# Performance work log

Measured on AMD Instinct MI355X. Metric: run time of the kernel, lower is better.

Reference implementation:

```python
import jax, jax.numpy as jnp
import numpy as np

B, T, J = 64, 1024, 22
PARENTS = [0, 0, 1, 2, 3, 0, 5, 6, 7, 0, 9, 10, 11, 12, 11, 14, 15, 16, 11, 18, 19, 20]
SPARSE_JOINTS = [0, 4, 8, 13, 17, 21]
EE = tuple(SPARSE_JOINTS[1:])                       # end effectors (sparse_joints[1:])
NO_SPARSE = tuple(j for j in range(J) if j not in SPARSE_JOINTS)
LAMBDA_EE, LAMBDA_EE_REG = 1.0, 0.1
IDENT_DQ = np.array([1, 0, 0, 0, 0, 0, 0, 0], dtype=np.float32)


def _qconj(q):
    return q * jnp.array([1.0, -1.0, -1.0, -1.0], q.dtype)


def _qmul(a, b):
    aw, ax, ay, az = a[..., 0], a[..., 1], a[..., 2], a[..., 3]
    bw, bx, by, bz = b[..., 0], b[..., 1], b[..., 2], b[..., 3]
    return jnp.stack([
        aw * bw - ax * bx - ay * by - az * bz,
        aw * bx + ax * bw + ay * bz - az * by,
        aw * by - ax * bz + ay * bw + az * bx,
        aw * bz + ax * by - ay * bx + az * bw], axis=-1)


def _qrot(q, v):
    # rotate vector v by unit quaternion q
    qv = q[..., 1:]
    t = 2.0 * jnp.cross(qv, v)
    return v + q[..., :1] * t + jnp.cross(qv, t)


def _qmat(q):
    w, x, y, z = q[..., 0], q[..., 1], q[..., 2], q[..., 3]
    m = jnp.stack([
        1 - 2 * (y * y + z * z), 2 * (x * y - w * z), 2 * (x * z + w * y),
        2 * (x * y + w * z), 1 - 2 * (x * x + z * z), 2 * (y * z - w * x),
        2 * (x * z - w * y), 2 * (y * z + w * x), 1 - 2 * (x * x + y * y)], axis=-1)
    return m.reshape(m.shape[:-1] + (3, 3))


def _denorm_to_dq(x, mean, std, set_root_identity):
    # x: (B, J*8, T) channel-major dual quats -> (B, T, J, 8)
    x = x * std[None, :, None] + mean[None, :, None]
    if set_root_identity:
        x = x.at[:, :8, :].set(jnp.asarray(IDENT_DQ, x.dtype)[None, :, None])
    b, c, t = x.shape
    return x.reshape(b, c // 8, 8, t).transpose(0, 3, 1, 2)


def _local_rot_from_dq(dq):
    # skeleton_from_dual_quat: real part = global rotation; make local via parent gather
    qr = dq[..., :4]
    qr = qr / jnp.linalg.norm(qr, axis=-1, keepdims=True)
    parent = jnp.asarray(PARENTS)
    local = _qmul(_qconj(qr[:, :, parent, :]), qr)   # (B,T,J,4)
    # forward_ik overwrites root local rotation with identity
    local = local.at[:, :, 0, :].set(jnp.array([1.0, 0.0, 0.0, 0.0], dq.dtype))
    return local


def _fk(local_rot, offsets):
    # fk_2: sequential parent-indexed propagation; root global pos is zeros
    rots = [local_rot[:, :, 0]]
    poss = [jnp.zeros(local_rot.shape[:2] + (3,), local_rot.dtype)]
    for j in range(1, J):
        p = PARENTS[j]
        rots.append(_qmul(rots[p], local_rot[:, :, j]))
        poss.append(_qrot(rots[p], offsets[j]) + poss[p])
    grot = jnp.stack(rots, axis=2)          # (B,T,J,4)
    pos = jnp.stack(poss, axis=2)           # (B,T,J,3)
    return pos, _qmat(grot)                  # positions, (B,T,J,3,3) rot matrices


def setup_inputs() -> dict:
    key = jax.random.key(0)
    ks = jax.random.split(key, 7)
    C = J * 8
    return {
        "input": jax.random.normal(ks[0], (B, C, T), jnp.float32),
        "input_ik": jax.random.normal(ks[1], (B, C - 8, T), jnp.float32),
        "input_decoder": jax.random.normal(ks[2], (B, C, T), jnp.float32),
        "target": jax.random.normal(ks[3], (B, C, T), jnp.float32),
        "mean_dqs": 0.1 * jax.random.normal(ks[4], (C,), jnp.float32),
        "std_dqs": 0.5 + 0.5 * jax.random.uniform(ks[5], (C,), jnp.float32),
        "offsets": jax.random.normal(ks[6], (J, 3), jnp.float32),
    }


def reference(input, input_ik, input_decoder, target, mean_dqs, std_dqs, offsets):
    # prepend identity-slot for the root (8 zero channels), then denormalize
    dq_ik = jnp.concatenate([jnp.zeros_like(input_ik[:, :8, :]), input_ik], axis=1)
    dq_ik = _denorm_to_dq(dq_ik, mean_dqs, std_dqs, True)
    dq_dec = _denorm_to_dq(input_decoder, mean_dqs, std_dqs, True)
    dq_tgt = _denorm_to_dq(target, mean_dqs, std_dqs, False)

    r_ik = _local_rot_from_dq(dq_ik)
    r_dec = _local_rot_from_dq(dq_dec)
    r_tgt = _local_rot_from_dq(dq_tgt)

    pos, rm = _fk(r_ik, offsets)
    tpos, trm = _fk(r_tgt, offsets)
    dpos, drm = _fk(r_dec, offsets)

    ee = jnp.asarray(EE)
    ns = jnp.asarray(NO_SPARSE)
    mse = lambda a, b: jnp.mean((a - b) ** 2)
    loss_ee = mse(pos[:, :, ee], tpos[:, :, ee]) + mse(rm[:, :, ee], trm[:, :, ee])
    loss_reg = mse(dpos[:, :, ns], pos[:, :, ns]) + mse(drm[:, :, ns], rm[:, :, ns])
    return loss_ee * LAMBDA_EE + loss_reg * LAMBDA_EE_REG
```

## Files before the change

### kernel.cpp

```cpp
#include <hip/hip_runtime.h>


#define T_DIM 1024

struct Q { float w, x, y, z; };
struct V3 { float x, y, z; };
struct St { Q rot; V3 pos; };

__device__ __forceinline__ Q qmul(const Q a, const Q b) {
    Q r;
    r.w = a.w*b.w - a.x*b.x - a.y*b.y - a.z*b.z;
    r.x = a.w*b.x + a.x*b.w + a.y*b.z - a.z*b.y;
    r.y = a.w*b.y - a.x*b.z + a.y*b.w + a.z*b.x;
    r.z = a.w*b.z + a.x*b.y - a.y*b.x + a.z*b.w;
    return r;
}

__device__ __forceinline__ V3 qrot(const Q q, const V3 v) {
    float tx = 2.f*(q.y*v.z - q.z*v.y);
    float ty = 2.f*(q.z*v.x - q.x*v.z);
    float tz = 2.f*(q.x*v.y - q.y*v.x);
    V3 r;
    r.x = v.x + q.w*tx + (q.y*tz - q.z*ty);
    r.y = v.y + q.w*ty + (q.z*tx - q.x*tz);
    r.z = v.z + q.w*tz + (q.x*ty - q.y*tx);
    return r;
}

__device__ __forceinline__ void qmat(const Q q, float m[9]) {
    float xx=q.x*q.x, yy=q.y*q.y, zz=q.z*q.z;
    float xy=q.x*q.y, xz=q.x*q.z, yz=q.y*q.z;
    float wx=q.w*q.x, wy=q.w*q.y, wz=q.w*q.z;
    m[0]=1.f-2.f*(yy+zz); m[1]=2.f*(xy-wz);     m[2]=2.f*(xz+wy);
    m[3]=2.f*(xy+wz);     m[4]=1.f-2.f*(xx+zz); m[5]=2.f*(yz-wx);
    m[6]=2.f*(xz-wy);     m[7]=2.f*(yz+wx);     m[8]=1.f-2.f*(xx+yy);
}

__device__ __forceinline__ float rmdiff2(const Q a, const Q b) {
    float ma[9], mb[9];
    qmat(a, ma); qmat(b, mb);
    float s = 0.f;
#pragma unroll
    for (int i = 0; i < 9; ++i) { float d = ma[i]-mb[i]; s += d*d; }
    return s;
}

__device__ __forceinline__ float pdiff2(const V3 a, const V3 b) {
    float dx=a.x-b.x, dy=a.y-b.y, dz=a.z-b.z;
    return dx*dx+dy*dy+dz*dz;
}

__device__ __forceinline__ V3 v3add(const V3 a, const V3 b) {
    return V3{a.x+b.x, a.y+b.y, a.z+b.z};
}

__device__ __forceinline__ Q mkq(const float r[4], const int c0,
                                 const float* __restrict__ mean,
                                 const float* __restrict__ stdv) {
    Q q;
    q.w = r[0]*stdv[c0+0] + mean[c0+0];
    q.x = r[1]*stdv[c0+1] + mean[c0+1];
    q.y = r[2]*stdv[c0+2] + mean[c0+2];
    q.z = r[3]*stdv[c0+3] + mean[c0+3];
    float inv = rsqrtf(q.w*q.w + q.x*q.x + q.y*q.y + q.z*q.z);
    q.w*=inv; q.x*=inv; q.y*=inv; q.z*=inv;
    return q;
}

template<int J0, int N>
__device__ __forceinline__ void prefetch_chain(
    const float* __restrict__ ikp, const float* __restrict__ dep,
    const float* __restrict__ tgp,
    float (*ikr)[4], float (*der)[4], float (*tgr)[4])
{
#pragma unroll
    for (int jj = 0; jj < N; ++jj) {
        const int j = J0 + jj;
#pragma unroll
        for (int c = 0; c < 4; ++c) {
            ikr[jj][c] = ikp[((j-1)*8 + c)*T_DIM];
            der[jj][c] = dep[(j*8 + c)*T_DIM];
            tgr[jj][c] = tgp[(j*8 + c)*T_DIM];
        }
    }
}

template<int J, bool EE>
__device__ __forceinline__ void stepr(
    St& sik, St& sde, St& stg,
    const float ikr[4], const float der[4], const float tgr[4],
    const float* __restrict__ mean, const float* __restrict__ stdv,
    const float* __restrict__ offs, const Q q0c,
    float& aep, float& aer, float& arp, float& arr)
{
    const int c0 = J*8;
    Q qik = mkq(ikr, c0, mean, stdv);
    Q qde = mkq(der, c0, mean, stdv);
    Q qtg = mkq(tgr, c0, mean, stdv);
    V3 off = { offs[3*J], offs[3*J+1], offs[3*J+2] };
    V3 pik = v3add(qrot(sik.rot, off), sik.pos);
    V3 pde = v3add(qrot(sde.rot, off), sde.pos);
    V3 ptg = v3add(qrot(stg.rot, off), stg.pos);
    Q rtg = qmul(q0c, qtg);
    if (EE) {
        aep += pdiff2(pik, ptg);
        aer += rmdiff2(qik, rtg);
    } else {
        arp += pdiff2(pde, pik);
        arr += rmdiff2(qde, qik);
    }
    sik.rot = qik; sik.pos = pik;
    sde.rot = qde; sde.pos = pde;
    stg.rot = rtg; stg.pos = ptg;
}

__global__ __launch_bounds__(256, 1) void fk_loss_kernel(
    const float* __restrict__ ik, const float* __restrict__ dec,
    const float* __restrict__ tgt, const float* __restrict__ mean,
    const float* __restrict__ stdv, const float* __restrict__ offs,
    float* __restrict__ out)
{
    __shared__ float swred[4];
    const int tid = threadIdx.x;
    const int p = blockIdx.x * 256 + tid;
    const int b = p >> 10;
    const int t = p & 1023;
    const float* ikp = ik  + (size_t)b * (168*1024) + t;
    const float* dep = dec + (size_t)b * (176*1024) + t;
    const float* tgp = tgt + (size_t)b * (176*1024) + t;

    float aep=0.f, aer=0.f, arp=0.f, arr=0.f;

    float Aik[4][4], Ade[4][4], Atg[4][4];
    float Bik[4][4], Bde[4][4], Btg[4][4];
    float Cik[5][4], Cde[5][4], Ctg[5][4];
    float Dik[4][4], Dde[4][4], Dtg[4][4];
    float Eik[4][4], Ede[4][4], Etg[4][4];
    float rq0[4];

#pragma unroll
    for (int c = 0; c < 4; ++c) rq0[c] = tgp[c*T_DIM];
    prefetch_chain<1,4>(ikp, dep, tgp, Aik, Ade, Atg);
    prefetch_chain<5,4>(ikp, dep, tgp, Bik, Bde, Btg);

    Q q0 = mkq(rq0, 0, mean, stdv);
    const Q q0c = { q0.w, -q0.x, -q0.y, -q0.z };
    const St root = { {1.f,0.f,0.f,0.f}, {0.f,0.f,0.f} };
    St sik, sde, stg;

    sik = root; sde = root; stg = root;
    stepr<1,false>(sik,sde,stg, Aik[0],Ade[0],Atg[0], mean,stdv,offs, q0c, aep,aer,arp,arr);
    stepr<2,false>(sik,sde,stg, Aik[1],Ade[1],Atg[1], mean,stdv,offs, q0c, aep,aer,arp,arr);
    stepr<3,false>(sik,sde,stg, Aik[2],Ade[2],Atg[2], mean,stdv,offs, q0c, aep,aer,arp,arr);
    stepr<4,true >(sik,sde,stg, Aik[3],Ade[3],Atg[3], mean,stdv,offs, q0c, aep,aer,arp,arr);

    prefetch_chain<9,5>(ikp, dep, tgp, Cik, Cde, Ctg);

    sik = root; sde = root; stg = root;
    stepr<5,false>(sik,sde,stg, Bik[0],Bde[0],Btg[0], mean,stdv,offs, q0c, aep,aer,arp,arr);
    stepr<6,false>(sik,sde,stg, Bik[1],Bde[1],Btg[1], mean,stdv,offs, q0c, aep,aer,arp,arr);
    stepr<7,false>(sik,sde,stg, Bik[2],Bde[2],Btg[2], mean,stdv,offs, q0c, aep,aer,arp,arr);
    stepr<8,true >(sik,sde,stg, Bik[3],Bde[3],Btg[3], mean,stdv,offs, q0c, aep,aer,arp,arr);

    prefetch_chain<14,4>(ikp, dep, tgp, Dik, Dde, Dtg);

    sik = root; sde = root; stg = root;
    stepr<9, false>(sik,sde,stg, Cik[0],Cde[0],Ctg[0], mean,stdv,offs, q0c, aep,aer,arp,arr);
    stepr<10,false>(sik,sde,stg, Cik[1],Cde[1],Ctg[1], mean,stdv,offs, q0c, aep,aer,arp,arr);
    stepr<11,false>(sik,sde,stg, Cik[2],Cde[2],Ctg[2], mean,stdv,offs, q0c, aep,aer,arp,arr);
    const St sik11 = sik, sde11 = sde, stg11 = stg;
    stepr<12,false>(sik,sde,stg, Cik[3],Cde[3],Ctg[3], mean,stdv,offs, q0c, aep,aer,arp,arr);
    stepr<13,true >(sik,sde,stg, Cik[4],Cde[4],Ctg[4], mean,stdv,offs, q0c, aep,aer,arp,arr);

    prefetch_chain<18,4>(ikp, dep, tgp, Eik, Ede, Etg);

    sik = sik11; sde = sde11; stg = stg11;
    stepr<14,false>(sik,sde,stg, Dik[0],Dde[0],Dtg[0], mean,stdv,offs, q0c, aep,aer,arp,arr);
    stepr<15,false>(sik,sde,stg, Dik[1],Dde[1],Dtg[1], mean,stdv,offs, q0c, aep,aer,arp,arr);
    stepr<16,false>(sik,sde,stg, Dik[2],Dde[2],Dtg[2], mean,stdv,offs, q0c, aep,aer,arp,arr);
    stepr<17,true >(sik,sde,stg, Dik[3],Dde[3],Dtg[3], mean,stdv,offs, q0c, aep,aer,arp,arr);

    sik = sik11; sde = sde11; stg = stg11;
    stepr<18,false>(sik,sde,stg, Eik[0],Ede[0],Etg[0], mean,stdv,offs, q0c, aep,aer,arp,arr);
    stepr<19,false>(sik,sde,stg, Eik[1],Ede[1],Etg[1], mean,stdv,offs, q0c, aep,aer,arp,arr);
    stepr<20,false>(sik,sde,stg, Eik[2],Ede[2],Etg[2], mean,stdv,offs, q0c, aep,aer,arp,arr);
    stepr<21,true >(sik,sde,stg, Eik[3],Ede[3],Etg[3], mean,stdv,offs, q0c, aep,aer,arp,arr);

    const float BT = 65536.f;
    float loss = aep * (1.0f/(BT*15.f))
               + aer * (1.0f/(BT*45.f))
               + arp * (0.1f/(BT*48.f))
               + arr * (0.1f/(BT*144.f));

#pragma unroll
    for (int o = 32; o > 0; o >>= 1) loss += __shfl_down(loss, o);
    if ((tid & 63) == 0) swred[tid >> 6] = loss;
    __syncthreads();
    if (tid == 0) {
        atomicAdd(out, swred[0]+swred[1]+swred[2]+swred[3]);
    }
}

extern "C" void kernel_launch(void* const* d_in, const int* in_sizes, int n_in,
                              void* d_out, int out_size, void* d_ws, size_t ws_size,
                              hipStream_t stream) {
    const float* ikx  = (const float*)d_in[1];
    const float* dec  = (const float*)d_in[2];
    const float* tgt  = (const float*)d_in[3];
    const float* mean = (const float*)d_in[4];
    const float* stdv = (const float*)d_in[5];
    const float* offs = (const float*)d_in[6];
    float* out = (float*)d_out;

    hipMemsetAsync(out, 0, sizeof(float), stream);
    fk_loss_kernel<<<256, 256, 0, stream>>>(ikx, dec, tgt, mean, stdv, offs, out);
}
```

Measured before the change: 173.0 us.

## Split FK loss into two thread roles and use closed-form rotation-matrix distance

Each block now has 512 threads: half compute the end-effector loss (ik vs target FK), the other half compute the regularizer (decoder vs ik FK). Each thread tracks two chains instead of three, which cuts register pressure and doubles the parallelism over the same 256 blocks. The ik chain is therefore computed twice, once per role. The 9-element rotation-matrix squared difference is replaced by the identity 8(1 - (a·b)^2) for unit quaternions, which drops the matrix construction.

```diff
diff --git a/kernel.cpp b/kernel.cpp
--- a/kernel.cpp
+++ b/kernel.cpp
@@ -27,22 +27,9 @@
     return r;
 }
 
-__device__ __forceinline__ void qmat(const Q q, float m[9]) {
-    float xx=q.x*q.x, yy=q.y*q.y, zz=q.z*q.z;
-    float xy=q.x*q.y, xz=q.x*q.z, yz=q.y*q.z;
-    float wx=q.w*q.x, wy=q.w*q.y, wz=q.w*q.z;
-    m[0]=1.f-2.f*(yy+zz); m[1]=2.f*(xy-wz);     m[2]=2.f*(xz+wy);
-    m[3]=2.f*(xy+wz);     m[4]=1.f-2.f*(xx+zz); m[5]=2.f*(yz-wx);
-    m[6]=2.f*(xz-wy);     m[7]=2.f*(yz+wx);     m[8]=1.f-2.f*(xx+yy);
-}
-
-__device__ __forceinline__ float rmdiff2(const Q a, const Q b) {
-    float ma[9], mb[9];
-    qmat(a, ma); qmat(b, mb);
-    float s = 0.f;
-#pragma unroll
-    for (int i = 0; i < 9; ++i) { float d = ma[i]-mb[i]; s += d*d; }
-    return s;
+__device__ __forceinline__ float rmdiff2u(const Q a, const Q b) {
+    float d = a.w*b.w + a.x*b.x + a.y*b.y + a.z*b.z;
+    return 8.f*(1.f - d*d);
 }
 
 __device__ __forceinline__ float pdiff2(const V3 a, const V3 b) {
@@ -68,136 +55,149 @@
 }
 
 template<int J0, int N>
-__device__ __forceinline__ void prefetch_chain(
-    const float* __restrict__ ikp, const float* __restrict__ dep,
-    const float* __restrict__ tgp,
-    float (*ikr)[4], float (*der)[4], float (*tgr)[4])
+__device__ __forceinline__ void pf2(
+    const float* __restrict__ xp, const float* __restrict__ yp,
+    float (*xr)[4], float (*yr)[4])
 {
 #pragma unroll
     for (int jj = 0; jj < N; ++jj) {
         const int j = J0 + jj;
 #pragma unroll
         for (int c = 0; c < 4; ++c) {
-            ikr[jj][c] = ikp[((j-1)*8 + c)*T_DIM];
-            der[jj][c] = dep[(j*8 + c)*T_DIM];
-            tgr[jj][c] = tgp[(j*8 + c)*T_DIM];
+            xr[jj][c] = xp[(j*8 + c)*T_DIM];
+            yr[jj][c] = yp[(j*8 + c)*T_DIM];
         }
     }
 }
 
-template<int J, bool EE>
-__device__ __forceinline__ void stepr(
-    St& sik, St& sde, St& stg,
-    const float ikr[4], const float der[4], const float tgr[4],
+template<int J, bool LOSS, bool PRE>
+__device__ __forceinline__ void step2(
+    St& sx, St& sy,
+    const float xr[4], const float yr[4],
     const float* __restrict__ mean, const float* __restrict__ stdv,
     const float* __restrict__ offs, const Q q0c,
-    float& aep, float& aer, float& arp, float& arr)
+    float& ap, float& ar)
 {
     const int c0 = J*8;
-    Q qik = mkq(ikr, c0, mean, stdv);
-    Q qde = mkq(der, c0, mean, stdv);
-    Q qtg = mkq(tgr, c0, mean, stdv);
+    Q qx = mkq(xr, c0, mean, stdv);
+    Q qy = mkq(yr, c0, mean, stdv);
+    if (PRE) qy = qmul(q0c, qy);
     V3 off = { offs[3*J], offs[3*J+1], offs[3*J+2] };
-    V3 pik = v3add(qrot(sik.rot, off), sik.pos);
-    V3 pde = v3add(qrot(sde.rot, off), sde.pos);
-    V3 ptg = v3add(qrot(stg.rot, off), stg.pos);
-    Q rtg = qmul(q0c, qtg);
-    if (EE) {
-        aep += pdiff2(pik, ptg);
-        aer += rmdiff2(qik, rtg);
-    } else {
-        arp += pdiff2(pde, pik);
-        arr += rmdiff2(qde, qik);
-    }
-    sik.rot = qik; sik.pos = pik;
-    sde.rot = qde; sde.pos = pde;
-    stg.rot = rtg; stg.pos = ptg;
-}
-
-__global__ __launch_bounds__(256, 1) void fk_loss_kernel(
+    V3 px = v3add(qrot(sx.rot, off), sx.pos);
+    V3 py = v3add(qrot(sy.rot, off), sy.pos);
+    if (LOSS) {
+        ap += pdiff2(px, py);
+        ar += rmdiff2u(qx, qy);
+    }
+    sx.rot = qx; sx.pos = px;
+    sy.rot = qy; sy.pos = py;
+}
+
+template<bool EEROLE>
+__device__ __forceinline__ void walk(
+    const float* __restrict__ xp, const float* __restrict__ yp,
+    const float* __restrict__ mean, const float* __restrict__ stdv,
+    const float* __restrict__ offs,
+    float& ap, float& ar)
+{
+    float Xa[4][4], Ya[4][4];
+    float Xb[4][4], Yb[4][4];
+    float Xc[5][4], Yc[5][4];
+    float Xd[4][4], Yd[4][4];
+    float Xe[4][4], Ye[4][4];
+    float rq0[4];
+
+    if (EEROLE) {
+#pragma unroll
+        for (int c = 0; c < 4; ++c) rq0[c] = yp[c*T_DIM];
+    }
+    pf2<1,4>(xp, yp, Xa, Ya);
+    pf2<5,4>(xp, yp, Xb, Yb);
+
+    Q q0c = {1.f, 0.f, 0.f, 0.f};
+    if (EEROLE) {
+        Q q0 = mkq(rq0, 0, mean, stdv);
+        q0c = { q0.w, -q0.x, -q0.y, -q0.z };
+    }
+    const St root = { {1.f,0.f,0.f,0.f}, {0.f,0.f,0.f} };
+    St sx, sy;
+
+    sx = root; sy = root;
+    step2<1, !EEROLE, EEROLE>(sx,sy, Xa[0],Ya[0], mean,stdv,offs,q0c, ap,ar);
+    step2<2, !EEROLE, EEROLE>(sx,sy, Xa[1],Ya[1], mean,stdv,offs,q0c, ap,ar);
+    step2<3, !EEROLE, EEROLE>(sx,sy, Xa[2],Ya[2], mean,stdv,offs,q0c, ap,ar);
+    step2<4,  EEROLE, EEROLE>(sx,sy, Xa[3],Ya[3], mean,stdv,offs,q0c, ap,ar);
+
+    pf2<9,5>(xp, yp, Xc, Yc);
+
+    sx = root; sy = root;
+    step2<5, !EEROLE, EEROLE>(sx,sy, Xb[0],Yb[0], mean,stdv,offs,q0c, ap,ar);
+    step2<6, !EEROLE, EEROLE>(sx,sy, Xb[1],Yb[1], mean,stdv,offs,q0c, ap,ar);
+    step2<7, !EEROLE, EEROLE>(sx,sy, Xb[2],Yb[2], mean,stdv,offs,q0c, ap,ar);
+    step2<8,  EEROLE, EEROLE>(sx,sy, Xb[3],Yb[3], mean,stdv,offs,q0c, ap,ar);
+
+    pf2<14,4>(xp, yp, Xd, Yd);
+
+    sx = root; sy = root;
+    step2<9,  !EEROLE, EEROLE>(sx,sy, Xc[0],Yc[0], mean,stdv,offs,q0c, ap,ar);
+    step2<10, !EEROLE, EEROLE>(sx,sy, Xc[1],Yc[1], mean,stdv,offs,q0c, ap,ar);
+    step2<11, !EEROLE, EEROLE>(sx,sy, Xc[2],Yc[2], mean,stdv,offs,q0c, ap,ar);
+    const St sx11 = sx, sy11 = sy;
+    step2<12, !EEROLE, EEROLE>(sx,sy, Xc[3],Yc[3], mean,stdv,offs,q0c, ap,ar);
+    step2<13,  EEROLE, EEROLE>(sx,sy, Xc[4],Yc[4], mean,stdv,offs,q0c, ap,ar);
+
+    pf2<18,4>(xp, yp, Xe, Ye);
+
+    sx = sx11; sy = sy11;
+    step2<14, !EEROLE, EEROLE>(sx,sy, Xd[0],Yd[0], mean,stdv,offs,q0c, ap,ar);
+    step2<15, !EEROLE, EEROLE>(sx,sy, Xd[1],Yd[1], mean,stdv,offs,q0c, ap,ar);
+    step2<16, !EEROLE, EEROLE>(sx,sy, Xd[2],Yd[2], mean,stdv,offs,q0c, ap,ar);
+    step2<17,  EEROLE, EEROLE>(sx,sy, Xd[3],Yd[3], mean,stdv,offs,q0c, ap,ar);
+
+    sx = sx11; sy = sy11;
+    step2<18, !EEROLE, EEROLE>(sx,sy, Xe[0],Ye[0], mean,stdv,offs,q0c, ap,ar);
+    step2<19, !EEROLE, EEROLE>(sx,sy, Xe[1],Ye[1], mean,stdv,offs,q0c, ap,ar);
+    step2<20, !EEROLE, EEROLE>(sx,sy, Xe[2],Ye[2], mean,stdv,offs,q0c, ap,ar);
+    step2<21,  EEROLE, EEROLE>(sx,sy, Xe[3],Ye[3], mean,stdv,offs,q0c, ap,ar);
+}
+
+__global__ __launch_bounds__(512, 2) void fk_loss_kernel(
     const float* __restrict__ ik, const float* __restrict__ dec,
     const float* __restrict__ tgt, const float* __restrict__ mean,
     const float* __restrict__ stdv, const float* __restrict__ offs,
     float* __restrict__ out)
 {
-    __shared__ float swred[4];
+    __shared__ float swred[8];
     const int tid = threadIdx.x;
-    const int p = blockIdx.x * 256 + tid;
+    const int role = tid >> 8;
+    const int lt = tid & 255;
+    const int p = blockIdx.x * 256 + lt;
     const int b = p >> 10;
     const int t = p & 1023;
-    const float* ikp = ik  + (size_t)b * (168*1024) + t;
+    const float* ikp = ik  + (size_t)b * (168*1024) + t - (size_t)(8*T_DIM);
     const float* dep = dec + (size_t)b * (176*1024) + t;
     const float* tgp = tgt + (size_t)b * (176*1024) + t;
 
-    float aep=0.f, aer=0.f, arp=0.f, arr=0.f;
-
-    float Aik[4][4], Ade[4][4], Atg[4][4];
-    float Bik[4][4], Bde[4][4], Btg[4][4];
-    float Cik[5][4], Cde[5][4], Ctg[5][4];
-    float Dik[4][4], Dde[4][4], Dtg[4][4];
-    float Eik[4][4], Ede[4][4], Etg[4][4];
-    float rq0[4];
-
-#pragma unroll
-    for (int c = 0; c < 4; ++c) rq0[c] = tgp[c*T_DIM];
-    prefetch_chain<1,4>(ikp, dep, tgp, Aik, Ade, Atg);
-    prefetch_chain<5,4>(ikp, dep, tgp, Bik, Bde, Btg);
-
-    Q q0 = mkq(rq0, 0, mean, stdv);
-    const Q q0c = { q0.w, -q0.x, -q0.y, -q0.z };
-    const St root = { {1.f,0.f,0.f,0.f}, {0.f,0.f,0.f} };
-    St sik, sde, stg;
-
-    sik = root; sde = root; stg = root;
-    stepr<1,false>(sik,sde,stg, Aik[0],Ade[0],Atg[0], mean,stdv,offs, q0c, aep,aer,arp,arr);
-    stepr<2,false>(sik,sde,stg, Aik[1],Ade[1],Atg[1], mean,stdv,offs, q0c, aep,aer,arp,arr);
-    stepr<3,false>(sik,sde,stg, Aik[2],Ade[2],Atg[2], mean,stdv,offs, q0c, aep,aer,arp,arr);
-    stepr<4,true >(sik,sde,stg, Aik[3],Ade[3],Atg[3], mean,stdv,offs, q0c, aep,aer,arp,arr);
-
-    prefetch_chain<9,5>(ikp, dep, tgp, Cik, Cde, Ctg);
-
-    sik = root; sde = root; stg = root;
-    stepr<5,false>(sik,sde,stg, Bik[0],Bde[0],Btg[0], mean,stdv,offs, q0c, aep,aer,arp,arr);
-    stepr<6,false>(sik,sde,stg, Bik[1],Bde[1],Btg[1], mean,stdv,offs, q0c, aep,aer,arp,arr);
-    stepr<7,false>(sik,sde,stg, Bik[2],Bde[2],Btg[2], mean,stdv,offs, q0c, aep,aer,arp,arr);
-    stepr<8,true >(sik,sde,stg, Bik[3],Bde[3],Btg[3], mean,stdv,offs, q0c, aep,aer,arp,arr);
-
-    prefetch_chain<14,4>(ikp, dep, tgp, Dik, Dde, Dtg);
-
-    sik = root; sde = root; stg = root;
-    stepr<9, false>(sik,sde,stg, Cik[0],Cde[0],Ctg[0], mean,stdv,offs, q0c, aep,aer,arp,arr);
-    stepr<10,false>(sik,sde,stg, Cik[1],Cde[1],Ctg[1], mean,stdv,offs, q0c, aep,aer,arp,arr);
-    stepr<11,false>(sik,sde,stg, Cik[2],Cde[2],Ctg[2], mean,stdv,offs, q0c, aep,aer,arp,arr);
-    const St sik11 = sik, sde11 = sde, stg11 = stg;
-    stepr<12,false>(sik,sde,stg, Cik[3],Cde[3],Ctg[3], mean,stdv,offs, q0c, aep,aer,arp,arr);
-    stepr<13,true >(sik,sde,stg, Cik[4],Cde[4],Ctg[4], mean,stdv,offs, q0c, aep,aer,arp,arr);
-
-    prefetch_chain<18,4>(ikp, dep, tgp, Eik, Ede, Etg);
-
-    sik = sik11; sde = sde11; stg = stg11;
-    stepr<14,false>(sik,sde,stg, Dik[0],Dde[0],Dtg[0], mean,stdv,offs, q0c, aep,aer,arp,arr);
-    stepr<15,false>(sik,sde,stg, Dik[1],Dde[1],Dtg[1], mean,stdv,offs, q0c, aep,aer,arp,arr);
-    stepr<16,false>(sik,sde,stg, Dik[2],Dde[2],Dtg[2], mean,stdv,offs, q0c, aep,aer,arp,arr);
-    stepr<17,true >(sik,sde,stg, Dik[3],Dde[3],Dtg[3], mean,stdv,offs, q0c, aep,aer,arp,arr);
-
-    sik = sik11; sde = sde11; stg = stg11;
-    stepr<18,false>(sik,sde,stg, Eik[0],Ede[0],Etg[0], mean,stdv,offs, q0c, aep,aer,arp,arr);
-    stepr<19,false>(sik,sde,stg, Eik[1],Ede[1],Etg[1], mean,stdv,offs, q0c, aep,aer,arp,arr);
-    stepr<20,false>(sik,sde,stg, Eik[2],Ede[2],Etg[2], mean,stdv,offs, q0c, aep,aer,arp,arr);
-    stepr<21,true >(sik,sde,stg, Eik[3],Ede[3],Etg[3], mean,stdv,offs, q0c, aep,aer,arp,arr);
-
+    float ap = 0.f, ar = 0.f;
+    float loss;
     const float BT = 65536.f;
-    float loss = aep * (1.0f/(BT*15.f))
-               + aer * (1.0f/(BT*45.f))
-               + arp * (0.1f/(BT*48.f))
-               + arr * (0.1f/(BT*144.f));
+    if (role == 0) {
+        walk<true>(ikp, tgp, mean, stdv, offs, ap, ar);
+        loss = ap * (1.0f/(BT*15.f)) + ar * (1.0f/(BT*45.f));
+    } else {
+        walk<false>(dep, ikp, mean, stdv, offs, ap, ar);
+        loss = ap * (0.1f/(BT*48.f)) + ar * (0.1f/(BT*144.f));
+    }
 
 #pragma unroll
     for (int o = 32; o > 0; o >>= 1) loss += __shfl_down(loss, o);
     if ((tid & 63) == 0) swred[tid >> 6] = loss;
     __syncthreads();
     if (tid == 0) {
-        atomicAdd(out, swred[0]+swred[1]+swred[2]+swred[3]);
+        float s = 0.f;
+#pragma unroll
+        for (int i = 0; i < 8; ++i) s += swred[i];
+        atomicAdd(out, s);
     }
 }
 
@@ -213,5 +213,5 @@
     float* out = (float*)d_out;
 
     hipMemsetAsync(out, 0, sizeof(float), stream);
-    fk_loss_kernel<<<256, 256, 0, stream>>>(ikx, dec, tgt, mean, stdv, offs, out);
-}
+    fk_loss_kernel<<<256, 512, 0, stream>>>(ikx, dec, tgt, mean, stdv, offs, out);
+}
```

Result: slower. 196.9 us (+13.8%).
